# Optimization experiments

Hardware: AMD Instinct MI355X
Metric: run time of the kernel (lower is better)

Reference implementation:

```python
import jax, jax.numpy as jnp
import numpy as np

B, NHID, L = 8, 256, 2048
NHEAD, HEAD_DIM = 8, 64
D = NHEAD * HEAD_DIM          # 512, q/k/v channels
DO = NHEAD * NHID             # 2048, output channels of WO
WIN = 3                       # unfold_size


def setup_inputs() -> dict:
    key = jax.random.key(0)
    ks = jax.random.split(key, 5)
    s = 0.02
    return {
        "x": jax.random.normal(ks[0], (B, NHID, L, 1), dtype=jnp.float32),
        "Wq": jax.random.normal(ks[1], (NHID, D), dtype=jnp.float32) * s,
        "bq": jnp.zeros((D,), jnp.float32),
        "Wk": jax.random.normal(ks[2], (NHID, D), dtype=jnp.float32) * s,
        "bk": jnp.zeros((D,), jnp.float32),
        "Wv": jax.random.normal(ks[3], (NHID, D), dtype=jnp.float32) * s,
        "bv": jnp.zeros((D,), jnp.float32),
        "Wo": jax.random.normal(ks[4], (D, DO), dtype=jnp.float32) * s,
        "bo": jnp.zeros((DO,), jnp.float32),
    }


def reference(x, Wq, bq, Wk, bk, Wv, bv, Wo, bo):
    # x: [B, nhid, L, 1]. 1x1 Conv2D over channel dim == dense on last axis.
    b, nhid, l, _ = x.shape
    xt = x[..., 0].transpose(0, 2, 1)            # [B, L, nhid]
    q = xt @ Wq + bq                             # [B, L, D]
    k = xt @ Wk + bk
    v = xt @ Wv + bv

    def windows(t):
        # SAME-padded sliding window of size 3 over L (tf.image.extract_patches)
        tp = jnp.pad(t, ((0, 0), (1, 1), (0, 0)))
        return jnp.stack([tp[:, i:i + l] for i in range(WIN)], axis=2)  # [B, L, 3, D]

    # D splits as (nhead, head_dim) with nhead outer, matching the reshapes
    # [B, nhead, head_dim, ...] in the original.
    qr = q.reshape(b, l, NHEAD, HEAD_DIM)                  # [B, L, n, h]
    kw = windows(k).reshape(b, l, WIN, NHEAD, HEAD_DIM)    # [B, L, w, n, h]
    vw = windows(v).reshape(b, l, WIN, NHEAD, HEAD_DIM)

    scale = jnp.asarray(1.0 / np.sqrt(HEAD_DIM), x.dtype)
    scores = jnp.einsum('blnh,blwnh->blnw', qr, kw) * scale  # [B, L, n, w]
    alphas = jax.nn.softmax(scores, axis=-1)                 # softmax over window
    att = jnp.einsum('blnw,blwnh->blnh', alphas, vw)         # [B, L, n, h]
    att = att.reshape(b, l, NHEAD * HEAD_DIM)                # [B, L, D]

    out = att @ Wo + bo                                      # [B, L, nhead*nhid]
    return out.transpose(0, 2, 1)[..., None]                 # [B, nhead*nhid, L, 1]
```

## Files before the change

### kernel.cpp

```cpp
#include <hip/hip_runtime.h>
#include <cstdint>
#include <cmath>

#define B_    8
#define NHID_ 256
#define L_    2048
#define D_    512
#define DO_   2048
#define QKVN  1536

using u16    = unsigned short;
using short8 = __attribute__((ext_vector_type(8))) short;
using f32x4  = __attribute__((ext_vector_type(4))) float;

typedef __attribute__((address_space(1))) void gv_t;
typedef __attribute__((address_space(3))) void lv_t;

__device__ inline void llds16(const void* g, void* l) {
  __builtin_amdgcn_global_load_lds((const gv_t*)g, (lv_t*)l, 16, 0, 0);
}

__device__ inline u16 f32_to_bf16(float f) {
  unsigned u = __float_as_uint(f);
  u += 0x7fffu + ((u >> 16) & 1u);
  return (u16)(u >> 16);
}

__device__ inline void load8(const u16* p, float f[8]) {
  uint4 u = *reinterpret_cast<const uint4*>(p);
  f[0] = __uint_as_float(u.x << 16); f[1] = __uint_as_float(u.x & 0xffff0000u);
  f[2] = __uint_as_float(u.y << 16); f[3] = __uint_as_float(u.y & 0xffff0000u);
  f[4] = __uint_as_float(u.z << 16); f[5] = __uint_as_float(u.z & 0xffff0000u);
  f[6] = __uint_as_float(u.w << 16); f[7] = __uint_as_float(u.w & 0xffff0000u);
}

__global__ void transpose_cvt(const float* __restrict__ src, u16* __restrict__ dst,
                              int rows, int cols) {
  __shared__ float tile[32][33];
  src += (size_t)blockIdx.z * rows * cols;
  dst += (size_t)blockIdx.z * rows * cols;
  int c0 = blockIdx.x * 32, r0 = blockIdx.y * 32;
  int tx = threadIdx.x, ty = threadIdx.y;
#pragma unroll
  for (int i = 0; i < 4; ++i)
    tile[ty + i * 8][tx] = src[(size_t)(r0 + ty + i * 8) * cols + c0 + tx];
  __syncthreads();
#pragma unroll
  for (int i = 0; i < 4; ++i)
    dst[(size_t)(c0 + ty + i * 8) * rows + r0 + tx] = f32_to_bf16(tile[tx][ty + i * 8]);
}

__global__ void concat_bias(const float* __restrict__ bq, const float* __restrict__ bk,
                            const float* __restrict__ bv, float* __restrict__ bqkv) {
  int d = blockIdx.x * 256 + threadIdx.x;
  float v = (d < 512) ? bq[d] : (d < 1024 ? bk[d - 512] : bv[d - 1024]);
  bqkv[d] = v;
}

#define BM 128
#define BN 128
#define BK 64

template <int K>
__device__ inline void gemm_tile(const u16* __restrict__ gA, const u16* __restrict__ gB,
                                 int m0, int n0, u16* As, u16* Bs, f32x4 (&acc)[4][4]) {
  const int tid = threadIdx.x;
  const int wave = tid >> 6, lane = tid & 63;
  const int wm = wave >> 1, wn = wave & 1;
  const int lrow = lane >> 3;
  const int lcol = (lane & 7) * 8;
  const int fr = lane & 15;
  const int fq = (lane >> 4) * 8;

#pragma unroll
  for (int i = 0; i < 4; ++i)
#pragma unroll
    for (int j = 0; j < 4; ++j) acc[i][j] = f32x4{0.f, 0.f, 0.f, 0.f};

  for (int k0 = 0; k0 < K; k0 += BK) {
#pragma unroll
    for (int t = 0; t < 4; ++t) {
      int chunk = wave * 4 + t;
      int row = chunk * 8 + lrow;
      llds16(gA + (size_t)(m0 + row) * K + k0 + lcol, (char*)As + chunk * 1024);
      llds16(gB + (size_t)(n0 + row) * K + k0 + lcol, (char*)Bs + chunk * 1024);
    }
    __syncthreads();
#pragma unroll
    for (int ks = 0; ks < 2; ++ks) {
      short8 a[4], b[4];
#pragma unroll
      for (int mt = 0; mt < 4; ++mt)
        a[mt] = *(const short8*)(As + (wm * 64 + mt * 16 + fr) * BK + ks * 32 + fq);
#pragma unroll
      for (int nt = 0; nt < 4; ++nt)
        b[nt] = *(const short8*)(Bs + (wn * 64 + nt * 16 + fr) * BK + ks * 32 + fq);
#pragma unroll
      for (int mt = 0; mt < 4; ++mt)
#pragma unroll
        for (int nt = 0; nt < 4; ++nt)
          acc[mt][nt] = __builtin_amdgcn_mfma_f32_16x16x32_bf16(a[mt], b[nt], acc[mt][nt], 0, 0, 0);
    }
    __syncthreads();
  }
}

__global__ __launch_bounds__(256) void qkv_gemm(const u16* __restrict__ xb,
                                                const u16* __restrict__ wT,
                                                const float* __restrict__ bqkv,
                                                u16* __restrict__ qkv) {
  __shared__ __align__(16) u16 As[BM * BK];
  __shared__ __align__(16) u16 Bs[BN * BK];
  int m0 = blockIdx.y * BM, n0 = blockIdx.x * BN;
  f32x4 acc[4][4];
  gemm_tile<NHID_>(xb, wT, m0, n0, As, Bs, acc);
  const int lane = threadIdx.x & 63, wave = threadIdx.x >> 6;
  const int wm = wave >> 1, wn = wave & 1;
#pragma unroll
  for (int mt = 0; mt < 4; ++mt) {
    int row0 = m0 + wm * 64 + mt * 16 + (lane >> 4) * 4;
#pragma unroll
    for (int nt = 0; nt < 4; ++nt) {
      int col = n0 + wn * 64 + nt * 16 + (lane & 15);
      float bias = bqkv[col];
#pragma unroll
      for (int r = 0; r < 4; ++r)
        qkv[(size_t)(row0 + r) * QKVN + col] = f32_to_bf16(acc[mt][nt][r] + bias);
    }
  }
}

__global__ __launch_bounds__(256) void out_gemm(const u16* __restrict__ woT,
                                                const u16* __restrict__ att,
                                                const float* __restrict__ bo,
                                                float* __restrict__ out) {
  __shared__ __align__(16) u16 As[BM * BK];
  __shared__ __align__(16) u16 Bs[BN * BK];
  int b = blockIdx.z;
  int m0 = blockIdx.y * BM;
  int n0 = blockIdx.x * BN;
  const u16* gB = att + (size_t)b * L_ * D_;
  f32x4 acc[4][4];
  gemm_tile<D_>(woT, gB, m0, n0, As, Bs, acc);
  const int lane = threadIdx.x & 63, wave = threadIdx.x >> 6;
  const int wm = wave >> 1, wn = wave & 1;
  float* outb = out + (size_t)b * DO_ * L_;
#pragma unroll
  for (int mt = 0; mt < 4; ++mt) {
    int row0 = m0 + wm * 64 + mt * 16 + (lane >> 4) * 4;
#pragma unroll
    for (int r = 0; r < 4; ++r) {
      float bias = bo[row0 + r];
#pragma unroll
      for (int nt = 0; nt < 4; ++nt) {
        int col = n0 + wn * 64 + nt * 16 + (lane & 15);
        outb[(size_t)(row0 + r) * L_ + col] = acc[mt][nt][r] + bias;
      }
    }
  }
}

__global__ __launch_bounds__(256) void attn_kernel(const u16* __restrict__ qkv,
                                                   u16* __restrict__ att) {
  const int wave = threadIdx.x >> 6, lane = threadIdx.x & 63;
  const int bl = blockIdx.x * 4 + wave;
  const int l = bl & (L_ - 1);
  const int c0 = (lane >> 3) * 64 + (lane & 7) * 8;

  float q[8];
  load8(qkv + (size_t)bl * QKVN + c0, q);

  float kk[3][8], vv[3][8];
#pragma unroll
  for (int w = 0; w < 3; ++w) {
    int lw = l + w - 1;
    if (lw >= 0 && lw < L_) {
      const u16* base = qkv + (size_t)(bl + w - 1) * QKVN;
      load8(base + 512 + c0, kk[w]);
      load8(base + 1024 + c0, vv[w]);
    } else {
#pragma unroll
      for (int t = 0; t < 8; ++t) { kk[w][t] = 0.f; vv[w][t] = 0.f; }
    }
  }

  float s[3];
#pragma unroll
  for (int w = 0; w < 3; ++w) {
    float a = 0.f;
#pragma unroll
    for (int t = 0; t < 8; ++t) a = fmaf(q[t], kk[w][t], a);
    s[w] = a;
  }
#pragma unroll
  for (int off = 1; off < 8; off <<= 1) {
    s[0] += __shfl_xor(s[0], off);
    s[1] += __shfl_xor(s[1], off);
    s[2] += __shfl_xor(s[2], off);
  }
  s[0] *= 0.125f; s[1] *= 0.125f; s[2] *= 0.125f;

  float mx = fmaxf(s[0], fmaxf(s[1], s[2]));
  float e0 = __expf(s[0] - mx), e1 = __expf(s[1] - mx), e2 = __expf(s[2] - mx);
  float inv = 1.f / (e0 + e1 + e2);
  float a0 = e0 * inv, a1 = e1 * inv, a2 = e2 * inv;

  u16 o16[8];
#pragma unroll
  for (int t = 0; t < 8; ++t) {
    float o = a0 * vv[0][t] + a1 * vv[1][t] + a2 * vv[2][t];
    o16[t] = f32_to_bf16(o);
  }
  uint4 pk;
  pk.x = (unsigned)o16[0] | ((unsigned)o16[1] << 16);
  pk.y = (unsigned)o16[2] | ((unsigned)o16[3] << 16);
  pk.z = (unsigned)o16[4] | ((unsigned)o16[5] << 16);
  pk.w = (unsigned)o16[6] | ((unsigned)o16[7] << 16);
  *reinterpret_cast<uint4*>(att + (size_t)bl * D_ + c0) = pk;
}

extern "C" void kernel_launch(void* const* d_in, const int* in_sizes, int n_in,
                              void* d_out, int out_size, void* d_ws, size_t ws_size,
                              hipStream_t stream) {
  const float* x  = (const float*)d_in[0];
  const float* Wq = (const float*)d_in[1];
  const float* bq = (const float*)d_in[2];
  const float* Wk = (const float*)d_in[3];
  const float* bk = (const float*)d_in[4];
  const float* Wv = (const float*)d_in[5];
  const float* bv = (const float*)d_in[6];
  const float* Wo = (const float*)d_in[7];
  const float* bo = (const float*)d_in[8];
  float* out = (float*)d_out;

  char* ws = (char*)d_ws;
  u16*   xb    = (u16*)(ws + 0);
  u16*   wqkvT = (u16*)(ws + 8388608);
  u16*   woT   = (u16*)(ws + 9175040);
  float* bqkv  = (float*)(ws + 11272192);
  u16*   qkv   = (u16*)(ws + 11278336);
  u16*   att   = (u16*)(ws + 61609984);

  dim3 tb(32, 8);
  transpose_cvt<<<dim3(L_ / 32, NHID_ / 32, B_), tb, 0, stream>>>(x, xb, NHID_, L_);
  transpose_cvt<<<dim3(D_ / 32, NHID_ / 32, 1), tb, 0, stream>>>(Wq, wqkvT, NHID_, D_);
  transpose_cvt<<<dim3(D_ / 32, NHID_ / 32, 1), tb, 0, stream>>>(Wk, wqkvT + 512 * NHID_, NHID_, D_);
  transpose_cvt<<<dim3(D_ / 32, NHID_ / 32, 1), tb, 0, stream>>>(Wv, wqkvT + 1024 * NHID_, NHID_, D_);
  transpose_cvt<<<dim3(DO_ / 32, D_ / 32, 1), tb, 0, stream>>>(Wo, woT, D_, DO_);
  concat_bias<<<QKVN / 256, 256, 0, stream>>>(bq, bk, bv, bqkv);

  qkv_gemm<<<dim3(QKVN / BN, (B_ * L_) / BM), 256, 0, stream>>>(xb, wqkvT, bqkv, qkv);

  attn_kernel<<<(B_ * L_) / 4, 256, 0, stream>>>(qkv, att);

  out_gemm<<<dim3(L_ / BN, DO_ / BM, B_), 256, 0, stream>>>(woT, att, bo, out);
}
```

Baseline: 253.7 us.

## Merge preprocessing launches into one kernel and XOR-swizzle GEMM LDS tiles

Replaces the six separate transpose and bias-concat launches with a single prep kernel that dispatches on block index, cutting launch overhead and tail gaps. The GEMM tile loader now applies an XOR swizzle to the k-chunk position when writing to LDS and reading fragments, to avoid LDS bank conflicts on the MFMA operand reads. The first tile load is also issued before the accumulator initialisation, and the loop is restructured so the final iteration skips the trailing barrier. The swizzle depends on the row-within-8 and the fragment row matching, so the indexing must stay consistent.

```diff
diff --git a/kernel.cpp b/kernel.cpp
--- a/kernel.cpp
+++ b/kernel.cpp
@@ -34,27 +34,58 @@
   f[6] = __uint_as_float(u.w << 16); f[7] = __uint_as_float(u.w & 0xffff0000u);
 }
 
-__global__ void transpose_cvt(const float* __restrict__ src, u16* __restrict__ dst,
-                              int rows, int cols) {
+template <int R, int C>
+__device__ inline void t32(const float* __restrict__ src, u16* __restrict__ dst,
+                           int id, float (*tile)[33]) {
+  constexpr int TPR = C / 32;
+  constexpr int PER = (R / 32) * TPR;
+  int z = id / PER, rem = id % PER;
+  int ry = rem / TPR, cx = rem % TPR;
+  src += (size_t)z * R * C;
+  dst += (size_t)z * R * C;
+  int c0 = cx * 32, r0 = ry * 32;
+  int tx = threadIdx.x, ty = threadIdx.y;
+#pragma unroll
+  for (int i = 0; i < 4; ++i)
+    tile[ty + i * 8][tx] = src[(size_t)(r0 + ty + i * 8) * C + c0 + tx];
+  __syncthreads();
+#pragma unroll
+  for (int i = 0; i < 4; ++i)
+    dst[(size_t)(c0 + ty + i * 8) * R + r0 + tx] = f32_to_bf16(tile[tx][ty + i * 8]);
+}
+
+#define PREP_X0   0
+#define PREP_WQ   4096
+#define PREP_WK   4224
+#define PREP_WV   4352
+#define PREP_WO   4480
+#define PREP_BIAS 5504
+#define PREP_NB   5510
+
+__global__ void prep_all(const float* __restrict__ x,
+                         const float* __restrict__ Wq, const float* __restrict__ Wk,
+                         const float* __restrict__ Wv, const float* __restrict__ Wo,
+                         const float* __restrict__ bq, const float* __restrict__ bk,
+                         const float* __restrict__ bv,
+                         u16* __restrict__ xb, u16* __restrict__ wqkvT,
+                         u16* __restrict__ woT, float* __restrict__ bqkv) {
   __shared__ float tile[32][33];
-  src += (size_t)blockIdx.z * rows * cols;
-  dst += (size_t)blockIdx.z * rows * cols;
-  int c0 = blockIdx.x * 32, r0 = blockIdx.y * 32;
-  int tx = threadIdx.x, ty = threadIdx.y;
-#pragma unroll
-  for (int i = 0; i < 4; ++i)
-    tile[ty + i * 8][tx] = src[(size_t)(r0 + ty + i * 8) * cols + c0 + tx];
-  __syncthreads();
-#pragma unroll
-  for (int i = 0; i < 4; ++i)
-    dst[(size_t)(c0 + ty + i * 8) * rows + r0 + tx] = f32_to_bf16(tile[tx][ty + i * 8]);
-}
-
-__global__ void concat_bias(const float* __restrict__ bq, const float* __restrict__ bk,
-                            const float* __restrict__ bv, float* __restrict__ bqkv) {
-  int d = blockIdx.x * 256 + threadIdx.x;
-  float v = (d < 512) ? bq[d] : (d < 1024 ? bk[d - 512] : bv[d - 1024]);
-  bqkv[d] = v;
+  int bid = blockIdx.x;
+  if (bid < PREP_WQ) {
+    t32<NHID_, L_>(x, xb, bid, tile);
+  } else if (bid < PREP_WK) {
+    t32<NHID_, D_>(Wq, wqkvT, bid - PREP_WQ, tile);
+  } else if (bid < PREP_WV) {
+    t32<NHID_, D_>(Wk, wqkvT + 512 * NHID_, bid - PREP_WK, tile);
+  } else if (bid < PREP_WO) {
+    t32<NHID_, D_>(Wv, wqkvT + 1024 * NHID_, bid - PREP_WV, tile);
+  } else if (bid < PREP_BIAS) {
+    t32<D_, DO_>(Wo, woT, bid - PREP_WO, tile);
+  } else {
+    int d = (bid - PREP_BIAS) * 256 + threadIdx.y * 32 + threadIdx.x;
+    float v = (d < 512) ? bq[d] : (d < 1024 ? bk[d - 512] : bv[d - 1024]);
+    bqkv[d] = v;
+  }
 }
 
 #define BM 128
@@ -67,41 +98,50 @@
   const int tid = threadIdx.x;
   const int wave = tid >> 6, lane = tid & 63;
   const int wm = wave >> 1, wn = wave & 1;
-  const int lrow = lane >> 3;
-  const int lcol = (lane & 7) * 8;
+  const int r8 = lane >> 3;
+  const int kc = ((lane & 7) ^ r8) * 8;
   const int fr = lane & 15;
-  const int fq = (lane >> 4) * 8;
-
-#pragma unroll
-  for (int i = 0; i < 4; ++i)
-#pragma unroll
-    for (int j = 0; j < 4; ++j) acc[i][j] = f32x4{0.f, 0.f, 0.f, 0.f};
-
-  for (int k0 = 0; k0 < K; k0 += BK) {
+  const int fx = fr & 7;
+  const int kq = lane >> 4;
+
+  auto stage = [&](int k0) {
 #pragma unroll
     for (int t = 0; t < 4; ++t) {
       int chunk = wave * 4 + t;
-      int row = chunk * 8 + lrow;
-      llds16(gA + (size_t)(m0 + row) * K + k0 + lcol, (char*)As + chunk * 1024);
-      llds16(gB + (size_t)(n0 + row) * K + k0 + lcol, (char*)Bs + chunk * 1024);
-    }
+      int row = chunk * 8 + r8;
+      llds16(gA + (size_t)(m0 + row) * K + k0 + kc, (char*)As + chunk * 1024);
+      llds16(gB + (size_t)(n0 + row) * K + k0 + kc, (char*)Bs + chunk * 1024);
+    }
+  };
+
+  stage(0);
+#pragma unroll
+  for (int i = 0; i < 4; ++i)
+#pragma unroll
+    for (int j = 0; j < 4; ++j) acc[i][j] = f32x4{0.f, 0.f, 0.f, 0.f};
+
+  for (int k0 = 0;;) {
     __syncthreads();
 #pragma unroll
     for (int ks = 0; ks < 2; ++ks) {
       short8 a[4], b[4];
+      const int slot = (((ks * 4 + kq) ^ fx)) * 8;
 #pragma unroll
       for (int mt = 0; mt < 4; ++mt)
-        a[mt] = *(const short8*)(As + (wm * 64 + mt * 16 + fr) * BK + ks * 32 + fq);
+        a[mt] = *(const short8*)(As + (wm * 64 + mt * 16 + fr) * BK + slot);
 #pragma unroll
       for (int nt = 0; nt < 4; ++nt)
-        b[nt] = *(const short8*)(Bs + (wn * 64 + nt * 16 + fr) * BK + ks * 32 + fq);
+        b[nt] = *(const short8*)(Bs + (wn * 64 + nt * 16 + fr) * BK + slot);
 #pragma unroll
       for (int mt = 0; mt < 4; ++mt)
 #pragma unroll
         for (int nt = 0; nt < 4; ++nt)
           acc[mt][nt] = __builtin_amdgcn_mfma_f32_16x16x32_bf16(a[mt], b[nt], acc[mt][nt], 0, 0, 0);
     }
+    k0 += BK;
+    if (k0 >= K) break;
     __syncthreads();
+    stage(k0);
   }
 }
 
@@ -241,13 +281,8 @@
   u16*   qkv   = (u16*)(ws + 11278336);
   u16*   att   = (u16*)(ws + 61609984);
 
-  dim3 tb(32, 8);
-  transpose_cvt<<<dim3(L_ / 32, NHID_ / 32, B_), tb, 0, stream>>>(x, xb, NHID_, L_);
-  transpose_cvt<<<dim3(D_ / 32, NHID_ / 32, 1), tb, 0, stream>>>(Wq, wqkvT, NHID_, D_);
-  transpose_cvt<<<dim3(D_ / 32, NHID_ / 32, 1), tb, 0, stream>>>(Wk, wqkvT + 512 * NHID_, NHID_, D_);
-  transpose_cvt<<<dim3(D_ / 32, NHID_ / 32, 1), tb, 0, stream>>>(Wv, wqkvT + 1024 * NHID_, NHID_, D_);
-  transpose_cvt<<<dim3(DO_ / 32, D_ / 32, 1), tb, 0, stream>>>(Wo, woT, D_, DO_);
-  concat_bias<<<QKVN / 256, 256, 0, stream>>>(bq, bk, bv, bqkv);
+  prep_all<<<PREP_NB, dim3(32, 8), 0, stream>>>(x, Wq, Wk, Wv, Wo, bq, bk, bv,
+                                                xb, wqkvT, woT, bqkv);
 
   qkv_gemm<<<dim3(QKVN / BN, (B_ * L_) / BM), 256, 0, stream>>>(xb, wqkvT, bqkv, qkv);
 
```

New measurement: 228.1 us. 1.11x faster.
